# Kernel optimization log

Measured on AMD Instinct MI355X. Metric: run time of the kernel, lower is better.

## Reference

```python
import jax, jax.numpy as jnp
import numpy as np

N_A = N_B = N_C = 50000
E = 800000
D_IN = 256
D_OUT = 128
T_ATT = 64


def _spmm(row, col, val, ft, n_dst):
    # sparse [n_dst, n_src] @ ft : gather src rows, scale, scatter-add to dst
    return jax.ops.segment_sum(val[:, None] * ft[col], row, num_segments=n_dst)


def setup_inputs() -> dict:
    key = jax.random.key(0)
    ks = jax.random.split(key, 40)
    f32 = jnp.float32
    inp = {
        'x_a': jax.random.normal(ks[0], (N_A, D_IN), f32),
        'x_b': jax.random.normal(ks[1], (N_B, D_IN), f32),
        'x_c': jax.random.normal(ks[2], (N_C, D_IN), f32),
    }
    # COO adjacency per relation: (dst_row, src_col, value)
    rel = {'ab': (N_A, N_B), 'ac': (N_A, N_C), 'ba': (N_B, N_A), 'ca': (N_C, N_A)}
    i = 3
    for name, (nd, ns) in rel.items():
        inp['row_' + name] = jax.random.randint(ks[i], (E,), 0, nd); i += 1
        inp['col_' + name] = jax.random.randint(ks[i], (E,), 0, ns); i += 1
        inp['val_' + name] = jax.random.uniform(ks[i], (E,), f32); i += 1
    # learned parameters (xavier-ish scale)
    def w(k, shape, s=0.05):
        return jax.random.normal(k, shape, f32) * s
    inp['w_self_a'] = w(ks[i], (D_IN, D_OUT)); i += 1
    inp['w_self_b'] = w(ks[i], (D_IN, D_OUT)); i += 1
    inp['w_self_c'] = w(ks[i], (D_IN, D_OUT)); i += 1
    inp['W_ab'] = w(ks[i], (D_IN, D_OUT)); i += 1
    inp['W_ac'] = w(ks[i], (D_IN, D_OUT)); i += 1
    inp['W_ba'] = w(ks[i], (D_IN, D_OUT)); i += 1
    inp['W_ca'] = w(ks[i], (D_IN, D_OUT)); i += 1
    inp['bias_a'] = w(ks[i], (1, D_OUT)); i += 1
    inp['bias_b'] = w(ks[i], (1, D_OUT)); i += 1
    inp['bias_c'] = w(ks[i], (1, D_OUT)); i += 1
    inp['w_cat_a'] = w(ks[i], (2 * D_OUT, D_OUT)); i += 1
    inp['w_cat_b'] = w(ks[i], (2 * D_OUT, D_OUT)); i += 1
    inp['w_cat_c'] = w(ks[i], (2 * D_OUT, D_OUT)); i += 1
    inp['w_query_a'] = w(ks[i], (D_OUT, T_ATT)); i += 1
    inp['w_keys_a'] = w(ks[i], (D_OUT, T_ATT)); i += 1
    inp['w_att_a'] = w(ks[i], (2 * T_ATT, 1)); i += 1
    return inp


def reference(x_a, x_b, x_c,
              row_ab, col_ab, val_ab, row_ac, col_ac, val_ac,
              row_ba, col_ba, val_ba, row_ca, col_ca, val_ca,
              w_self_a, w_self_b, w_self_c,
              W_ab, W_ac, W_ba, W_ca,
              bias_a, bias_b, bias_c,
              w_cat_a, w_cat_b, w_cat_c,
              w_query_a, w_keys_a, w_att_a):
    # ---- type 'a': neighbors [b, c], attention fusion ----
    self_a = x_a @ w_self_a                                   # [Na, D]
    nb_b = _spmm(row_ab, col_ab, val_ab, x_b @ W_ab, N_A)     # [Na, D]
    nb_c = _spmm(row_ac, col_ac, val_ac, x_c @ W_ac, N_A)     # [Na, D]
    q = self_a @ w_query_a                                    # [Na, T]
    e_b = jax.nn.elu(jnp.concatenate([nb_b @ w_keys_a, q], 1) @ w_att_a)  # [Na, 1]
    e_c = jax.nn.elu(jnp.concatenate([nb_c @ w_keys_a, q], 1) @ w_att_a)  # [Na, 1]
    att = jax.nn.softmax(jnp.concatenate([e_b, e_c], 1), axis=1)          # [Na, 2]
    agg_a = nb_b * att[:, :1] + nb_c * att[:, 1:2]
    out_a = jnp.concatenate([agg_a, self_a], 1) @ w_cat_a + bias_a
    # ---- type 'b': single neighbor 'a' ----
    self_b = x_b @ w_self_b
    agg_b = _spmm(row_ba, col_ba, val_ba, x_a @ W_ba, N_B)
    out_b = jnp.concatenate([agg_b, self_b], 1) @ w_cat_b + bias_b
    # ---- type 'c': single neighbor 'a' ----
    self_c = x_c @ w_self_c
    agg_c = _spmm(row_ca, col_ca, val_ca, x_a @ W_ca, N_C)
    out_c = jnp.concatenate([agg_c, self_c], 1) @ w_cat_c + bias_c
    # concat per-type outputs (all D_OUT wide) into one array
    return jnp.concatenate([out_a, out_b, out_c], 0)          # [Na+Nb+Nc, D]
```

## Files before the change

kernel.cpp:

```cpp
#include <hip/hip_runtime.h>

#define NA 50000
#define NE 800000
#define NBKT 196
#define CAP 4608
#define BSTRIDE (NBKT * CAP)

typedef unsigned int   u32;
typedef unsigned short u16;
typedef short s16x8 __attribute__((ext_vector_type(8)));
typedef float f32x4 __attribute__((ext_vector_type(4)));

__device__ __forceinline__ u16 f2bf(float f) {
  u32 u = __float_as_uint(f);
  u += 0x7fffu + ((u >> 16) & 1u);
  return (u16)(u >> 16);
}

__device__ __forceinline__ void acc8(float* a, uint4 q, float v) {
  a[0] += v * __uint_as_float(q.x << 16);
  a[1] += v * __uint_as_float(q.x & 0xffff0000u);
  a[2] += v * __uint_as_float(q.y << 16);
  a[3] += v * __uint_as_float(q.y & 0xffff0000u);
  a[4] += v * __uint_as_float(q.z << 16);
  a[5] += v * __uint_as_float(q.z & 0xffff0000u);
  a[6] += v * __uint_as_float(q.w << 16);
  a[7] += v * __uint_as_float(q.w & 0xffff0000u);
}

struct Rel4 { const int* row[4]; const int* col[4]; const float* val[4]; };

struct Prep {
  const float* src[10]; u16* dst[10];
  const float* wq; const float* wk; const float* wa; float* uvp;
  u32* gcur;
};

struct FtArgs { const float* A[3]; const u16* Bt[3]; u16* C[3]; };

__global__ __launch_bounds__(256) void k_prep(Prep P) {
  int gy = blockIdx.y;
  if (gy < 10) {
    int idx = blockIdx.x * 256 + threadIdx.x;
    int k = idx & 255, n = idx >> 8;
    P.dst[gy][n * 256 + k] = f2bf(P.src[gy][k * 128 + n]);
  } else if (blockIdx.x == 0) {
    int t = threadIdx.x;
    int d = t & 127, which = t >> 7;
    const float* w = which ? P.wq : P.wk;
    const float* a = P.wa + which * 64;
    float s = 0.f;
    for (int i = 0; i < 64; ++i) s += w[d * 64 + i] * a[i];
    P.uvp[which * 128 + d] = s;
  } else if (blockIdx.x == 1) {
    for (int i = threadIdx.x; i < 1024; i += 256)
      P.gcur[i] = (u32)((i & 255) * CAP);
  }
}

__global__ __launch_bounds__(256) void k_main1(Rel4 R, u32* __restrict__ gcur,
                                               uint2* __restrict__ pairs, FtArgs Ar) {
  __shared__ __align__(16) char smem[40960];
  const int gy = blockIdx.y;
  const int t = threadIdx.x;
  if (gy < 4) {
    if (blockIdx.x >= 196) return;
    int rel = gy;
    int e0 = blockIdx.x * 4096;
    int nrem = min(4096, NE - e0);
    u32* sw0  = (u32*)smem;
    u32* sval = sw0 + 4096;
    unsigned char* sbkt = (unsigned char*)(sval + 4096);
    u32* hist  = (u32*)(sbkt + 4096);
    u32* lscan = hist + 256;
    u32* cnt2  = lscan + 256;
    u32* gbase = cnt2 + 256;
    hist[t] = 0; cnt2[t] = 0;
    __syncthreads();
    const int* rr = R.row[rel];
    const int* cc = R.col[rel];
    const float* vl = R.val[rel];
    u32 w0[16]; u32 vv[16]; int bb[16];
    #pragma unroll
    for (int i = 0; i < 16; ++i) {
      int li = t + i * 256;
      bool ok = li < nrem;
      int idx = e0 + (ok ? li : 0);
      int r = ok ? rr[idx] : 0;
      int c = ok ? cc[idx] : 0;
      float v = ok ? vl[idx] : 0.f;
      u32 b = (u32)r >> 8;
      w0[i] = (u32)(c & 0xFFFF) | ((u32)(r & 255) << 16) | (b << 24);
      vv[i] = __float_as_uint(v);
      bb[i] = ok ? (int)b : -1;
      if (ok) atomicAdd(&hist[b], 1u);
    }
    __syncthreads();
    lscan[t] = hist[t];
    __syncthreads();
    for (int ofs = 1; ofs < 256; ofs <<= 1) {
      u32 y = (t >= ofs) ? lscan[t - ofs] : 0u;
      __syncthreads();
      lscan[t] += y;
      __syncthreads();
    }
    gbase[t] = atomicAdd(&gcur[rel * 256 + t], hist[t]);
    #pragma unroll
    for (int i = 0; i < 16; ++i) {
      if (bb[i] >= 0) {
        int b = bb[i];
        u32 p = (lscan[b] - hist[b]) + atomicAdd(&cnt2[b], 1u);
        sw0[p] = w0[i]; sval[p] = vv[i]; sbkt[p] = (unsigned char)b;
      }
    }
    __syncthreads();
    uint2* P = pairs + (size_t)rel * BSTRIDE;
    #pragma unroll
    for (int i = 0; i < 16; ++i) {
      int p = t + i * 256;
      if (p < nrem) {
        int b = sbkt[p];
        u32 gd = gbase[b] + (u32)p - (lscan[b] - hist[b]);
        uint2 pr; pr.x = sw0[p]; pr.y = sval[p];
        P[gd] = pr;
      }
    }
  } else {
    u16* Al = (u16*)smem;
    u16* Bl = Al + 128 * 72;
    const int by = gy - 4;
    const int which = (by < 3) ? 0 : (by < 5 ? 1 : 2);
    const int col0 = (by - (which == 0 ? 0 : (which == 1 ? 3 : 5))) * 128;
    const int ldc = (which == 0) ? 384 : 256;
    const float* A = Ar.A[which];
    const u16* Bt = Ar.Bt[which] + (size_t)col0 * 256;
    u16* C = Ar.C[which] + col0;
    const int row0 = blockIdx.x * 128;
    const int w = t >> 6, l = t & 63;
    const int wr = (w >> 1) * 64, wc = (w & 1) * 64;
    const int sr = t >> 1, kb = (t & 1) * 32;
    f32x4 acc[4][4] = {};
    for (int kk = 0; kk < 4; ++kk) {
      if (row0 + sr < NA) {
        const float* ap = A + (size_t)(row0 + sr) * 256 + kk * 64 + kb;
        #pragma unroll
        for (int h = 0; h < 2; ++h) {
          float f[16];
          #pragma unroll
          for (int i = 0; i < 4; ++i) {
            float4 v4 = *(const float4*)(ap + h * 16 + i * 4);
            f[4*i] = v4.x; f[4*i+1] = v4.y; f[4*i+2] = v4.z; f[4*i+3] = v4.w;
          }
          s16x8 v0, v1;
          #pragma unroll
          for (int i = 0; i < 8; ++i) { v0[i] = (short)f2bf(f[i]); v1[i] = (short)f2bf(f[i + 8]); }
          *(s16x8*)&Al[sr * 72 + kb + h * 16]     = v0;
          *(s16x8*)&Al[sr * 72 + kb + h * 16 + 8] = v1;
        }
      } else {
        s16x8 z = {0,0,0,0,0,0,0,0};
        #pragma unroll
        for (int h = 0; h < 4; ++h) *(s16x8*)&Al[sr * 72 + kb + h * 8] = z;
      }
      {
        const u16* bp = Bt + (size_t)sr * 256 + kk * 64 + kb;
        #pragma unroll
        for (int h = 0; h < 4; ++h)
          *(s16x8*)&Bl[sr * 72 + kb + h * 8] = *(const s16x8*)(bp + h * 8);
      }
      __syncthreads();
      #pragma unroll
      for (int ks = 0; ks < 2; ++ks) {
        s16x8 af[4], bfr[4];
        #pragma unroll
        for (int i = 0; i < 4; ++i)
          af[i] = *(const s16x8*)&Al[(wr + i * 16 + (l & 15)) * 72 + ks * 32 + (l >> 4) * 8];
        #pragma unroll
        for (int j = 0; j < 4; ++j)
          bfr[j] = *(const s16x8*)&Bl[(wc + j * 16 + (l & 15)) * 72 + ks * 32 + (l >> 4) * 8];
        #pragma unroll
        for (int i = 0; i < 4; ++i)
          #pragma unroll
          for (int j = 0; j < 4; ++j)
            acc[i][j] = __builtin_amdgcn_mfma_f32_16x16x32_bf16(af[i], bfr[j], acc[i][j], 0, 0, 0);
      }
      __syncthreads();
    }
    #pragma unroll
    for (int i = 0; i < 4; ++i)
      #pragma unroll
      for (int j = 0; j < 4; ++j)
        #pragma unroll
        for (int q = 0; q < 4; ++q) {
          int r = row0 + wr + i * 16 + (l >> 4) * 4 + q;
          if (r < NA) C[(size_t)r * ldc + wc + j * 16 + (l & 15)] = f2bf(acc[i][j][q]);
        }
  }
}

__global__ __launch_bounds__(256) void k_binB(const u32* __restrict__ gcur,
    int* __restrict__ ofs_s, int* __restrict__ ofs_e,
    const uint2* __restrict__ pairs, u32* __restrict__ epak) {
  int rel = blockIdx.y;
  int b = blockIdx.x;
  int base = b * CAP;
  int n = (int)gcur[rel * 256 + b] - base;
  __shared__ u32 sw0[CAP];
  __shared__ u32 sv[CAP];
  __shared__ u32 hist[256], scan[256], cur[256];
  int t = threadIdx.x;
  hist[t] = 0;
  __syncthreads();
  const uint2* P = pairs + (size_t)rel * BSTRIDE;
  for (int p = t; p < n; p += 256) {
    uint2 pr = P[base + p];
    sw0[p] = pr.x; sv[p] = pr.y;
    atomicAdd(&hist[(pr.x >> 16) & 255], 1u);
  }
  __syncthreads();
  u32 own = hist[t];
  scan[t] = own;
  __syncthreads();
  for (int ofs = 1; ofs < 256; ofs <<= 1) {
    u32 y = (t >= ofs) ? scan[t - ofs] : 0u;
    __syncthreads();
    scan[t] += y;
    __syncthreads();
  }
  u32 excl = scan[t] - own;
  cur[t] = excl;
  int r0 = b << 8;
  if (r0 + t < NA) {
    ofs_s[(size_t)rel * NA + r0 + t] = base + (int)excl;
    ofs_e[(size_t)rel * NA + r0 + t] = base + (int)(excl + own);
  }
  __syncthreads();
  u32* E = epak + (size_t)rel * BSTRIDE;
  for (int p = t; p < n; p += 256) {
    u32 w = sw0[p];
    int rl = (w >> 16) & 255;
    u32 d = atomicAdd(&cur[rl], 1u);
    E[base + (int)d] = (w & 0xFFFFu) | ((u32)f2bf(__uint_as_float(sv[p])) << 16);
  }
}

__global__ __launch_bounds__(256) void k_spmm(
    const int* __restrict__ ofs_s, const int* __restrict__ ofs_e,
    const u32* __restrict__ epak,
    const u16* __restrict__ ya, const u16* __restrict__ yb, const u16* __restrict__ yc,
    const float* __restrict__ uv,
    u16* __restrict__ agg_a, u16* __restrict__ agg_b, u16* __restrict__ agg_c) {
  int tid = threadIdx.x;
  int lane = tid & 63, wid = tid >> 6;
  int g = lane >> 4, gl = lane & 15;
  int row = blockIdx.x * 16 + wid * 4 + g;
  int gy = blockIdx.y;
  if (gy == 0) {
    float fb[8] = {0,0,0,0,0,0,0,0};
    float fc[8] = {0,0,0,0,0,0,0,0};
    {
      const u32* pr = epak;
      int i = ofs_s[row], e = ofs_e[row];
      for (; i + 4 <= e; i += 4) {
        u32 p0 = pr[i], p1 = pr[i + 1], p2 = pr[i + 2], p3 = pr[i + 3];
        uint4 q0 = *(const uint4*)((const u32*)(yb + (size_t)(p0 & 0xFFFFu) * 256) + gl * 4);
        uint4 q1 = *(const uint4*)((const u32*)(yb + (size_t)(p1 & 0xFFFFu) * 256) + gl * 4);
        uint4 q2 = *(const uint4*)((const u32*)(yb + (size_t)(p2 & 0xFFFFu) * 256) + gl * 4);
        uint4 q3 = *(const uint4*)((const u32*)(yb + (size_t)(p3 & 0xFFFFu) * 256) + gl * 4);
        acc8(fb, q0, __uint_as_float(p0 & 0xffff0000u));
        acc8(fb, q1, __uint_as_float(p1 & 0xffff0000u));
        acc8(fb, q2, __uint_as_float(p2 & 0xffff0000u));
        acc8(fb, q3, __uint_as_float(p3 & 0xffff0000u));
      }
      for (; i < e; ++i) {
        u32 p0 = pr[i];
        uint4 q0 = *(const uint4*)((const u32*)(yb + (size_t)(p0 & 0xFFFFu) * 256) + gl * 4);
        acc8(fb, q0, __uint_as_float(p0 & 0xffff0000u));
      }
    }
    {
      const u32* pr = epak + (size_t)BSTRIDE;
      int i = ofs_s[NA + row], e = ofs_e[NA + row];
      for (; i + 4 <= e; i += 4) {
        u32 p0 = pr[i], p1 = pr[i + 1], p2 = pr[i + 2], p3 = pr[i + 3];
        uint4 q0 = *(const uint4*)((const u32*)(yc + (size_t)(p0 & 0xFFFFu) * 256) + gl * 4);
        uint4 q1 = *(const uint4*)((const u32*)(yc + (size_t)(p1 & 0xFFFFu) * 256) + gl * 4);
        uint4 q2 = *(const uint4*)((const u32*)(yc + (size_t)(p2 & 0xFFFFu) * 256) + gl * 4);
        uint4 q3 = *(const uint4*)((const u32*)(yc + (size_t)(p3 & 0xFFFFu) * 256) + gl * 4);
        acc8(fc, q0, __uint_as_float(p0 & 0xffff0000u));
        acc8(fc, q1, __uint_as_float(p1 & 0xffff0000u));
        acc8(fc, q2, __uint_as_float(p2 & 0xffff0000u));
        acc8(fc, q3, __uint_as_float(p3 & 0xffff0000u));
      }
      for (; i < e; ++i) {
        u32 p0 = pr[i];
        uint4 q0 = *(const uint4*)((const u32*)(yc + (size_t)(p0 & 0xFFFFu) * 256) + gl * 4);
        acc8(fc, q0, __uint_as_float(p0 & 0xffff0000u));
      }
    }
    float sf[8];
    {
      uint4 sq = *(const uint4*)((const u32*)(ya + (size_t)row * 384) + gl * 4);
      sf[0] = __uint_as_float(sq.x << 16); sf[1] = __uint_as_float(sq.x & 0xffff0000u);
      sf[2] = __uint_as_float(sq.y << 16); sf[3] = __uint_as_float(sq.y & 0xffff0000u);
      sf[4] = __uint_as_float(sq.z << 16); sf[5] = __uint_as_float(sq.z & 0xffff0000u);
      sf[6] = __uint_as_float(sq.w << 16); sf[7] = __uint_as_float(sq.w & 0xffff0000u);
    }
    float pb = 0.f, pc = 0.f, pq = 0.f;
    const float* up = uv + gl * 8;
    const float* vp = uv + 128 + gl * 8;
    #pragma unroll
    for (int j = 0; j < 8; ++j) {
      pb += fb[j] * up[j];
      pc += fc[j] * up[j];
      pq += sf[j] * vp[j];
    }
    #pragma unroll
    for (int off = 1; off < 16; off <<= 1) {
      pb += __shfl_xor(pb, off);
      pc += __shfl_xor(pc, off);
      pq += __shfl_xor(pq, off);
    }
    float eb = pb + pq, ec = pc + pq;
    eb = eb > 0.f ? eb : (expf(eb) - 1.f);
    ec = ec > 0.f ? ec : (expf(ec) - 1.f);
    float m = fmaxf(eb, ec);
    float p0 = expf(eb - m), p1 = expf(ec - m);
    float inv = 1.f / (p0 + p1);
    float a0 = p0 * inv, a1 = p1 * inv;
    uint4 o;
    o.x = (u32)f2bf(a0 * fb[0] + a1 * fc[0]) | ((u32)f2bf(a0 * fb[1] + a1 * fc[1]) << 16);
    o.y = (u32)f2bf(a0 * fb[2] + a1 * fc[2]) | ((u32)f2bf(a0 * fb[3] + a1 * fc[3]) << 16);
    o.z = (u32)f2bf(a0 * fb[4] + a1 * fc[4]) | ((u32)f2bf(a0 * fb[5] + a1 * fc[5]) << 16);
    o.w = (u32)f2bf(a0 * fb[6] + a1 * fc[6]) | ((u32)f2bf(a0 * fb[7] + a1 * fc[7]) << 16);
    *(uint4*)((u32*)(agg_a + (size_t)row * 128) + gl * 4) = o;
  } else {
    int which = gy - 1;
    const int* os = ofs_s + (2 + which) * NA;
    const int* oe = ofs_e + (2 + which) * NA;
    const u32* pr = epak + (size_t)(2 + which) * BSTRIDE;
    const u16* ft = ya + (which ? 256 : 128);
    u16* agg = which ? agg_c : agg_b;
    float fa[8] = {0,0,0,0,0,0,0,0};
    int i = os[row], e = oe[row];
    for (; i + 4 <= e; i += 4) {
      u32 p0 = pr[i], p1 = pr[i + 1], p2 = pr[i + 2], p3 = pr[i + 3];
      uint4 q0 = *(const uint4*)((const u32*)(ft + (size_t)(p0 & 0xFFFFu) * 384) + gl * 4);
      uint4 q1 = *(const uint4*)((const u32*)(ft + (size_t)(p1 & 0xFFFFu) * 384) + gl * 4);
      uint4 q2 = *(const uint4*)((const u32*)(ft + (size_t)(p2 & 0xFFFFu) * 384) + gl * 4);
      uint4 q3 = *(const uint4*)((const u32*)(ft + (size_t)(p3 & 0xFFFFu) * 384) + gl * 4);
      acc8(fa, q0, __uint_as_float(p0 & 0xffff0000u));
      acc8(fa, q1, __uint_as_float(p1 & 0xffff0000u));
      acc8(fa, q2, __uint_as_float(p2 & 0xffff0000u));
      acc8(fa, q3, __uint_as_float(p3 & 0xffff0000u));
    }
    for (; i < e; ++i) {
      u32 p0 = pr[i];
      uint4 q0 = *(const uint4*)((const u32*)(ft + (size_t)(p0 & 0xFFFFu) * 384) + gl * 4);
      acc8(fa, q0, __uint_as_float(p0 & 0xffff0000u));
    }
    uint4 o;
    o.x = (u32)f2bf(fa[0]) | ((u32)f2bf(fa[1]) << 16);
    o.y = (u32)f2bf(fa[2]) | ((u32)f2bf(fa[3]) << 16);
    o.z = (u32)f2bf(fa[4]) | ((u32)f2bf(fa[5]) << 16);
    o.w = (u32)f2bf(fa[6]) | ((u32)f2bf(fa[7]) << 16);
    *(uint4*)((u32*)(agg + (size_t)row * 128) + gl * 4) = o;
  }
}

struct OutArgs {
  const u16* Agg[3]; const u16* Self[3]; int lds_[3];
  const u16* Bt[3]; const float* bias[3]; float* Out[3];
};

__global__ __launch_bounds__(256) void k_gemm_out(OutArgs Ar) {
  __shared__ u16 Al[128 * 72];
  __shared__ u16 Bl[128 * 72];
  const int which = blockIdx.y;
  const u16* Agg = Ar.Agg[which];
  const u16* Self = Ar.Self[which];
  const int ldself = Ar.lds_[which];
  const u16* Bt = Ar.Bt[which];
  const float* bias = Ar.bias[which];
  float* Out = Ar.Out[which];
  const int row0 = blockIdx.x * 128;
  const int t = threadIdx.x;
  const int w = t >> 6, l = t & 63;
  const int wr = (w >> 1) * 64, wc = (w & 1) * 64;
  const int sr = t >> 1, kb = (t & 1) * 32;
  f32x4 acc[4][4] = {};
  for (int kk = 0; kk < 4; ++kk) {
    {
      const u16* sp = (kk < 2) ? (Agg + (size_t)(row0 + sr) * 128 + kk * 64 + kb)
                               : (Self + (size_t)(row0 + sr) * ldself + (kk - 2) * 64 + kb);
      if (row0 + sr < NA) {
        #pragma unroll
        for (int h = 0; h < 4; ++h)
          *(s16x8*)&Al[sr * 72 + kb + h * 8] = *(const s16x8*)(sp + h * 8);
      } else {
        s16x8 z = {0,0,0,0,0,0,0,0};
        #pragma unroll
        for (int h = 0; h < 4; ++h) *(s16x8*)&Al[sr * 72 + kb + h * 8] = z;
      }
    }
    {
      const u16* bp = Bt + (size_t)sr * 256 + kk * 64 + kb;
      #pragma unroll
      for (int h = 0; h < 4; ++h)
        *(s16x8*)&Bl[sr * 72 + kb + h * 8] = *(const s16x8*)(bp + h * 8);
    }
    __syncthreads();
    #pragma unroll
    for (int ks = 0; ks < 2; ++ks) {
      s16x8 af[4], bfr[4];
      #pragma unroll
      for (int i = 0; i < 4; ++i)
        af[i] = *(const s16x8*)&Al[(wr + i * 16 + (l & 15)) * 72 + ks * 32 + (l >> 4) * 8];
      #pragma unroll
      for (int j = 0; j < 4; ++j)
        bfr[j] = *(const s16x8*)&Bl[(wc + j * 16 + (l & 15)) * 72 + ks * 32 + (l >> 4) * 8];
      #pragma unroll
      for (int i = 0; i < 4; ++i)
        #pragma unroll
        for (int j = 0; j < 4; ++j)
          acc[i][j] = __builtin_amdgcn_mfma_f32_16x16x32_bf16(af[i], bfr[j], acc[i][j], 0, 0, 0);
    }
    __syncthreads();
  }
  #pragma unroll
  for (int i = 0; i < 4; ++i)
    #pragma unroll
    for (int j = 0; j < 4; ++j)
      #pragma unroll
      for (int q = 0; q < 4; ++q) {
        int r = row0 + wr + i * 16 + (l >> 4) * 4 + q;
        int c = wc + j * 16 + (l & 15);
        if (r < NA) Out[(size_t)r * 128 + c] = acc[i][j][q] + bias[c];
      }
}

extern "C" void kernel_launch(void* const* d_in, const int* in_sizes, int n_in,
                              void* d_out, int out_size, void* d_ws, size_t ws_size,
                              hipStream_t stream) {
  const float* x_a = (const float*)d_in[0];
  const float* x_b = (const float*)d_in[1];
  const float* x_c = (const float*)d_in[2];
  const int* row_ab = (const int*)d_in[3];
  const int* col_ab = (const int*)d_in[4];
  const float* val_ab = (const float*)d_in[5];
  const int* row_ac = (const int*)d_in[6];
  const int* col_ac = (const int*)d_in[7];
  const float* val_ac = (const float*)d_in[8];
  const int* row_ba = (const int*)d_in[9];
  const int* col_ba = (const int*)d_in[10];
  const float* val_ba = (const float*)d_in[11];
  const int* row_ca = (const int*)d_in[12];
  const int* col_ca = (const int*)d_in[13];
  const float* val_ca = (const float*)d_in[14];
  const float* w_self_a = (const float*)d_in[15];
  const float* w_self_b = (const float*)d_in[16];
  const float* w_self_c = (const float*)d_in[17];
  const float* W_ab = (const float*)d_in[18];
  const float* W_ac = (const float*)d_in[19];
  const float* W_ba = (const float*)d_in[20];
  const float* W_ca = (const float*)d_in[21];
  const float* bias_a = (const float*)d_in[22];
  const float* bias_b = (const float*)d_in[23];
  const float* bias_c = (const float*)d_in[24];
  const float* w_cat_a = (const float*)d_in[25];
  const float* w_cat_b = (const float*)d_in[26];
  const float* w_cat_c = (const float*)d_in[27];
  const float* w_query_a = (const float*)d_in[28];
  const float* w_keys_a = (const float*)d_in[29];
  const float* w_att_a = (const float*)d_in[30];

  float* out = (float*)d_out;

  char* ws = (char*)d_ws;
  size_t off_b = 0;
  auto walloc = [&](size_t bytes) {
    void* p = ws + off_b;
    off_b = (off_b + bytes + 255) & ~(size_t)255;
    return p;
  };
  u16* ya = (u16*)walloc((size_t)NA * 384 * 2);
  u16* yb = (u16*)walloc((size_t)NA * 256 * 2);
  u16* yc = (u16*)walloc((size_t)NA * 256 * 2);
  u16* agg_a = (u16*)walloc((size_t)NA * 128 * 2);
  u16* agg_b = (u16*)walloc((size_t)NA * 128 * 2);
  u16* agg_c = (u16*)walloc((size_t)NA * 128 * 2);
  int* ofs_s = (int*)walloc((size_t)4 * NA * 4);
  int* ofs_e = (int*)walloc((size_t)4 * NA * 4);
  u32* gcur = (u32*)walloc((size_t)4 * 256 * 4);
  uint2* pairs = (uint2*)walloc((size_t)4 * BSTRIDE * 8);
  u32* epak = (u32*)walloc((size_t)4 * BSTRIDE * 4);
  u16* Wa_t = (u16*)walloc((size_t)384 * 256 * 2);
  u16* Wb_t = (u16*)walloc((size_t)256 * 256 * 2);
  u16* Wc_t = (u16*)walloc((size_t)256 * 256 * 2);
  u16* Wcat_a = (u16*)walloc((size_t)128 * 256 * 2);
  u16* Wcat_b = (u16*)walloc((size_t)128 * 256 * 2);
  u16* Wcat_c = (u16*)walloc((size_t)128 * 256 * 2);
  float* uvbuf = (float*)walloc(256 * 4);

  Rel4 R;
  R.row[0] = row_ab; R.col[0] = col_ab; R.val[0] = val_ab;
  R.row[1] = row_ac; R.col[1] = col_ac; R.val[1] = val_ac;
  R.row[2] = row_ba; R.col[2] = col_ba; R.val[2] = val_ba;
  R.row[3] = row_ca; R.col[3] = col_ca; R.val[3] = val_ca;

  Prep P;
  P.src[0] = w_self_a; P.dst[0] = Wa_t;
  P.src[1] = W_ba;     P.dst[1] = Wa_t + 128 * 256;
  P.src[2] = W_ca;     P.dst[2] = Wa_t + 256 * 256;
  P.src[3] = W_ab;     P.dst[3] = Wb_t;
  P.src[4] = w_self_b; P.dst[4] = Wb_t + 128 * 256;
  P.src[5] = W_ac;     P.dst[5] = Wc_t;
  P.src[6] = w_self_c; P.dst[6] = Wc_t + 128 * 256;
  P.src[7] = w_cat_a;  P.dst[7] = Wcat_a;
  P.src[8] = w_cat_b;  P.dst[8] = Wcat_b;
  P.src[9] = w_cat_c;  P.dst[9] = Wcat_c;
  P.wq = w_query_a; P.wk = w_keys_a; P.wa = w_att_a; P.uvp = uvbuf;
  P.gcur = gcur;

  dim3 gp(128, 11);
  k_prep<<<gp, 256, 0, stream>>>(P);

  FtArgs FA;
  FA.A[0] = x_a; FA.A[1] = x_b; FA.A[2] = x_c;
  FA.Bt[0] = Wa_t; FA.Bt[1] = Wb_t; FA.Bt[2] = Wc_t;
  FA.C[0] = ya; FA.C[1] = yb; FA.C[2] = yc;
  dim3 g1(391, 11);
  k_main1<<<g1, 256, 0, stream>>>(R, gcur, pairs, FA);

  dim3 gB(NBKT, 4);
  k_binB<<<gB, 256, 0, stream>>>(gcur, ofs_s, ofs_e, pairs, epak);

  dim3 gs(3125, 3);
  k_spmm<<<gs, 256, 0, stream>>>(ofs_s, ofs_e, epak, ya, yb, yc, uvbuf,
                                 agg_a, agg_b, agg_c);

  OutArgs OA;
  OA.Agg[0] = agg_a; OA.Agg[1] = agg_b; OA.Agg[2] = agg_c;
  OA.Self[0] = ya; OA.Self[1] = yb + 128; OA.Self[2] = yc + 128;
  OA.lds_[0] = 384; OA.lds_[1] = 256; OA.lds_[2] = 256;
  OA.Bt[0] = Wcat_a; OA.Bt[1] = Wcat_b; OA.Bt[2] = Wcat_c;
  OA.bias[0] = bias_a; OA.bias[1] = bias_b; OA.bias[2] = bias_c;
  OA.Out[0] = out; OA.Out[1] = out + (size_t)NA * 128; OA.Out[2] = out + (size_t)NA * 128 * 2;
  dim3 go(391, 3);
  k_gemm_out<<<go, 256, 0, stream>>>(OA);
}
```

Baseline: 303.5 us.

## Pre-convert inputs to bf16 in binning pass and fuse bucket sort with feature GEMM

The fp32-to-bf16 conversion of the three node feature matrices moves out of the GEMM and into the first binning kernel as a separate elementwise pass writing a bf16 copy of x. The second-stage bucket sort (formerly its own kernel) is merged into the same launch as the feature GEMM, which now reads bf16 A directly. The aim is to overlap the sort with the GEMM and to halve the GEMM's A-side load bandwidth and conversion ALU work. In exchange it adds a full extra write and read of a 77 MB bf16 copy of the inputs.

```diff
diff --git a/kernel.cpp b/kernel.cpp
--- a/kernel.cpp
+++ b/kernel.cpp
@@ -36,7 +36,9 @@
   u32* gcur;
 };
 
-struct FtArgs { const float* A[3]; const u16* Bt[3]; u16* C[3]; };
+struct ConvArgs { const float* x[3]; u16* xb; };
+
+struct FtArgs { const u16* A[3]; const u16* Bt[3]; u16* C[3]; };
 
 __global__ __launch_bounds__(256) void k_prep(Prep P) {
   int gy = blockIdx.y;
@@ -59,7 +61,7 @@
 }
 
 __global__ __launch_bounds__(256) void k_main1(Rel4 R, u32* __restrict__ gcur,
-                                               uint2* __restrict__ pairs, FtArgs Ar) {
+                                               uint2* __restrict__ pairs, ConvArgs CA) {
   __shared__ __align__(16) char smem[40960];
   const int gy = blockIdx.y;
   const int t = threadIdx.x;
@@ -126,13 +128,87 @@
       }
     }
   } else {
+    const size_t TOT = 38400000;
+    const size_t TSZ = 12800000;
+    size_t base = ((size_t)(gy - 4) * 391 + blockIdx.x) * 16384 + (size_t)t * 8;
+    #pragma unroll
+    for (int it = 0; it < 8; ++it) {
+      size_t g = base + (size_t)it * 2048;
+      if (g < TOT) {
+        int which = (g >= 2 * TSZ) ? 2 : (g >= TSZ ? 1 : 0);
+        size_t off = g - (size_t)which * TSZ;
+        const float* sp = CA.x[which] + off;
+        float4 v0 = *(const float4*)(sp);
+        float4 v1 = *(const float4*)(sp + 4);
+        s16x8 o;
+        o[0] = (short)f2bf(v0.x); o[1] = (short)f2bf(v0.y);
+        o[2] = (short)f2bf(v0.z); o[3] = (short)f2bf(v0.w);
+        o[4] = (short)f2bf(v1.x); o[5] = (short)f2bf(v1.y);
+        o[6] = (short)f2bf(v1.z); o[7] = (short)f2bf(v1.w);
+        *(s16x8*)(CA.xb + g) = o;
+      }
+    }
+  }
+}
+
+__global__ __launch_bounds__(256) void k_main2(const u32* __restrict__ gcur,
+    int* __restrict__ ofs_s, int* __restrict__ ofs_e,
+    const uint2* __restrict__ pairs, u32* __restrict__ epak, FtArgs Ar) {
+  __shared__ __align__(16) char smem[40960];
+  const int gy = blockIdx.y;
+  const int t = threadIdx.x;
+  if (gy < 4) {
+    if (blockIdx.x >= 196) return;
+    int rel = gy;
+    int b = blockIdx.x;
+    int base = b * CAP;
+    int n = (int)gcur[rel * 256 + b] - base;
+    u32* sw0  = (u32*)smem;
+    u32* sv   = sw0 + CAP;
+    u32* hist = sv + CAP;
+    u32* scan = hist + 256;
+    u32* cur  = scan + 256;
+    hist[t] = 0;
+    __syncthreads();
+    const uint2* P = pairs + (size_t)rel * BSTRIDE;
+    for (int p = t; p < n; p += 256) {
+      uint2 pr = P[base + p];
+      sw0[p] = pr.x; sv[p] = pr.y;
+      atomicAdd(&hist[(pr.x >> 16) & 255], 1u);
+    }
+    __syncthreads();
+    u32 own = hist[t];
+    scan[t] = own;
+    __syncthreads();
+    for (int ofs = 1; ofs < 256; ofs <<= 1) {
+      u32 y = (t >= ofs) ? scan[t - ofs] : 0u;
+      __syncthreads();
+      scan[t] += y;
+      __syncthreads();
+    }
+    u32 excl = scan[t] - own;
+    cur[t] = excl;
+    int r0 = b << 8;
+    if (r0 + t < NA) {
+      ofs_s[(size_t)rel * NA + r0 + t] = base + (int)excl;
+      ofs_e[(size_t)rel * NA + r0 + t] = base + (int)(excl + own);
+    }
+    __syncthreads();
+    u32* E = epak + (size_t)rel * BSTRIDE;
+    for (int p = t; p < n; p += 256) {
+      u32 w = sw0[p];
+      int rl = (w >> 16) & 255;
+      u32 d = atomicAdd(&cur[rl], 1u);
+      E[base + (int)d] = (w & 0xFFFFu) | ((u32)f2bf(__uint_as_float(sv[p])) << 16);
+    }
+  } else {
     u16* Al = (u16*)smem;
     u16* Bl = Al + 128 * 72;
     const int by = gy - 4;
     const int which = (by < 3) ? 0 : (by < 5 ? 1 : 2);
     const int col0 = (by - (which == 0 ? 0 : (which == 1 ? 3 : 5))) * 128;
     const int ldc = (which == 0) ? 384 : 256;
-    const float* A = Ar.A[which];
+    const u16* A = Ar.A[which];
     const u16* Bt = Ar.Bt[which] + (size_t)col0 * 256;
     u16* C = Ar.C[which] + col0;
     const int row0 = blockIdx.x * 128;
@@ -142,21 +218,10 @@
     f32x4 acc[4][4] = {};
     for (int kk = 0; kk < 4; ++kk) {
       if (row0 + sr < NA) {
-        const float* ap = A + (size_t)(row0 + sr) * 256 + kk * 64 + kb;
-        #pragma unroll
-        for (int h = 0; h < 2; ++h) {
-          float f[16];
-          #pragma unroll
-          for (int i = 0; i < 4; ++i) {
-            float4 v4 = *(const float4*)(ap + h * 16 + i * 4);
-            f[4*i] = v4.x; f[4*i+1] = v4.y; f[4*i+2] = v4.z; f[4*i+3] = v4.w;
-          }
-          s16x8 v0, v1;
-          #pragma unroll
-          for (int i = 0; i < 8; ++i) { v0[i] = (short)f2bf(f[i]); v1[i] = (short)f2bf(f[i + 8]); }
-          *(s16x8*)&Al[sr * 72 + kb + h * 16]     = v0;
-          *(s16x8*)&Al[sr * 72 + kb + h * 16 + 8] = v1;
-        }
+        const u16* ap = A + (size_t)(row0 + sr) * 256 + kk * 64 + kb;
+        #pragma unroll
+        for (int h = 0; h < 4; ++h)
+          *(s16x8*)&Al[sr * 72 + kb + h * 8] = *(const s16x8*)(ap + h * 8);
       } else {
         s16x8 z = {0,0,0,0,0,0,0,0};
         #pragma unroll
@@ -195,52 +260,6 @@
           int r = row0 + wr + i * 16 + (l >> 4) * 4 + q;
           if (r < NA) C[(size_t)r * ldc + wc + j * 16 + (l & 15)] = f2bf(acc[i][j][q]);
         }
-  }
-}
-
-__global__ __launch_bounds__(256) void k_binB(const u32* __restrict__ gcur,
-    int* __restrict__ ofs_s, int* __restrict__ ofs_e,
-    const uint2* __restrict__ pairs, u32* __restrict__ epak) {
-  int rel = blockIdx.y;
-  int b = blockIdx.x;
-  int base = b * CAP;
-  int n = (int)gcur[rel * 256 + b] - base;
-  __shared__ u32 sw0[CAP];
-  __shared__ u32 sv[CAP];
-  __shared__ u32 hist[256], scan[256], cur[256];
-  int t = threadIdx.x;
-  hist[t] = 0;
-  __syncthreads();
-  const uint2* P = pairs + (size_t)rel * BSTRIDE;
-  for (int p = t; p < n; p += 256) {
-    uint2 pr = P[base + p];
-    sw0[p] = pr.x; sv[p] = pr.y;
-    atomicAdd(&hist[(pr.x >> 16) & 255], 1u);
-  }
-  __syncthreads();
-  u32 own = hist[t];
-  scan[t] = own;
-  __syncthreads();
-  for (int ofs = 1; ofs < 256; ofs <<= 1) {
-    u32 y = (t >= ofs) ? scan[t - ofs] : 0u;
-    __syncthreads();
-    scan[t] += y;
-    __syncthreads();
-  }
-  u32 excl = scan[t] - own;
-  cur[t] = excl;
-  int r0 = b << 8;
-  if (r0 + t < NA) {
-    ofs_s[(size_t)rel * NA + r0 + t] = base + (int)excl;
-    ofs_e[(size_t)rel * NA + r0 + t] = base + (int)(excl + own);
-  }
-  __syncthreads();
-  u32* E = epak + (size_t)rel * BSTRIDE;
-  for (int p = t; p < n; p += 256) {
-    u32 w = sw0[p];
-    int rl = (w >> 16) & 255;
-    u32 d = atomicAdd(&cur[rl], 1u);
-    E[base + (int)d] = (w & 0xFFFFu) | ((u32)f2bf(__uint_as_float(sv[p])) << 16);
   }
 }
 
@@ -501,6 +520,7 @@
   u16* Wcat_b = (u16*)walloc((size_t)128 * 256 * 2);
   u16* Wcat_c = (u16*)walloc((size_t)128 * 256 * 2);
   float* uvbuf = (float*)walloc(256 * 4);
+  u16* xb = (u16*)walloc((size_t)3 * NA * 256 * 2);
 
   Rel4 R;
   R.row[0] = row_ab; R.col[0] = col_ab; R.val[0] = val_ab;
@@ -525,15 +545,18 @@
   dim3 gp(128, 11);
   k_prep<<<gp, 256, 0, stream>>>(P);
 
+  ConvArgs CA;
+  CA.x[0] = x_a; CA.x[1] = x_b; CA.x[2] = x_c;
+  CA.xb = xb;
+  dim3 g1(391, 11);
+  k_main1<<<g1, 256, 0, stream>>>(R, gcur, pairs, CA);
+
   FtArgs FA;
-  FA.A[0] = x_a; FA.A[1] = x_b; FA.A[2] = x_c;
+  FA.A[0] = xb; FA.A[1] = xb + (size_t)NA * 256; FA.A[2] = xb + (size_t)2 * NA * 256;
   FA.Bt[0] = Wa_t; FA.Bt[1] = Wb_t; FA.Bt[2] = Wc_t;
   FA.C[0] = ya; FA.C[1] = yb; FA.C[2] = yc;
-  dim3 g1(391, 11);
-  k_main1<<<g1, 256, 0, stream>>>(R, gcur, pairs, FA);
-
-  dim3 gB(NBKT, 4);
-  k_binB<<<gB, 256, 0, stream>>>(gcur, ofs_s, ofs_e, pairs, epak);
+  dim3 g2(391, 11);
+  k_main2<<<g2, 256, 0, stream>>>(gcur, ofs_s, ofs_e, pairs, epak, FA);
 
   dim3 gs(3125, 3);
   k_spmm<<<gs, 256, 0, stream>>>(ofs_s, ofs_e, epak, ya, yb, yc, uvbuf,
```

New measurement: 308.3 us. About the same (+1.6%).
